# Optimization experiments

Hardware: AMD Instinct MI355X
Metric: run time of the kernel (lower is better)

## Reference

```python
import jax, jax.numpy as jnp
import numpy as np

D = 128; H = 4; DH = D // H; L = 2
NC = 50000; ND = 20000; NG = 30000; E = 200000; P = 200000
A = 10; S = 5; EAD = 32
# edge type table: (src node type, dst node type); node types: 0=chemical,1=disease,2=gene
ST = (0, 2, 0, 1, 1, 2)
DT = (2, 0, 1, 0, 2, 1)


def _seg_softmax(e, seg, n):
    # numerically stable softmax over edges grouped by destination node
    m = jax.ops.segment_max(e, seg, num_segments=n)
    ex = jnp.exp(e - m[seg])
    s = jax.ops.segment_sum(ex, seg, num_segments=n)
    return ex / (s[seg] + 1e-16)


def _ln(x, g, b):
    mu = jnp.mean(x, -1, keepdims=True)
    v = jnp.mean((x - mu) ** 2, -1, keepdims=True)
    return (x - mu) * jax.lax.rsqrt(v + 1e-5) * g + b


def setup_inputs():
    key = jax.random.key(0)
    ks = iter(jax.random.split(key, 80))
    nrm = lambda shape, sc: jax.random.normal(next(ks), shape, jnp.float32) * sc
    z = lambda shape: jnp.zeros(shape, jnp.float32)
    inp = {
        'emb_c': nrm((NC, D), 0.1), 'emb_d': nrm((ND, D), 0.1), 'emb_g': nrm((NG, D), 0.1),
        'Wsrc': nrm((L, 6, D, D), D ** -0.5), 'bsrc': z((L, 6, D)),
        'Wdst': nrm((L, 6, D, D), D ** -0.5), 'bdst': z((L, 6, D)),
        'attn': nrm((L, 6, H, DH), 0.1),
        'Wout': nrm((L, 3, D, D), D ** -0.5), 'bout': z((L, 3, D)),
        'ln_g': jnp.ones((L, 3, D), jnp.float32), 'ln_b': z((L, 3, D)),
        'at_emb': nrm((L, A, EAD), 0.1), 'as_emb': nrm((L, S, EAD), 0.1),
        'Wcat': nrm((L, 2, 2 * EAD, D), (2 * EAD) ** -0.5), 'bcat': z((L, 2, D)),
        'Wc1': nrm((L, 2, 2, D), 0.5), 'bc1': z((L, 2, D)),
        'Wc2': nrm((L, 2, D, D), D ** -0.5), 'bc2': z((L, 2, D)),
        'W_cd': nrm((D, D), D ** -0.5),
        'ea4': jax.random.normal(next(ks), (E, 2), jnp.float32),
        'ea5': jax.random.normal(next(ks), (E, 2), jnp.float32),
    }
    ri = lambda n: jax.random.randint(next(ks), (E,), 0, n)
    inp.update(src0=ri(NC), dst0=ri(NG), src1=ri(NG), dst1=ri(NC),
               src2=ri(NC), dst2=ri(ND), src3=ri(ND), dst3=ri(NC),
               src4=ri(ND), dst4=ri(NG), src5=ri(NG), dst5=ri(ND))
    inp['ea0'] = jnp.stack([ri(A), ri(S)], 1)
    inp['ea1'] = jnp.stack([ri(A), ri(S)], 1)
    inp['pair_src'] = jax.random.randint(next(ks), (P,), 0, NC)
    inp['pair_dst'] = jax.random.randint(next(ks), (P,), 0, ND)
    return inp


def _fwd(emb_c, emb_d, emb_g, Wsrc, bsrc, Wdst, bdst, attn, Wout, bout, ln_g, ln_b,
         at_emb, as_emb, Wcat, bcat, Wc1, bc1, Wc2, bc2, W_cd, ea4, ea5,
         SRC, DST, ea0, ea1, pair_src, pair_dst):
    xs = [emb_c, emb_d, emb_g]
    Ns = [x.shape[0] for x in xs]
    cat_attr = {0: ea0, 1: ea1}
    cont_attr = {4: ea4, 5: ea5}
    for l in range(L):
        agg = [jnp.zeros_like(x) for x in xs]
        for r in range(6):
            st, dt = ST[r], DT[r]
            si, di = SRC[r], DST[r]
            hs = xs[st] @ Wsrc[l, r] + bsrc[l, r]           # [Ns, D]
            hd = xs[dt] @ Wdst[l, r] + bdst[l, r]           # [Nd, D]
            ms = hs[si].reshape(-1, H, DH)                  # [E, H, DH] gathered src msgs
            md = hd[di].reshape(-1, H, DH)
            e = jax.nn.leaky_relu(jnp.sum((ms + md) * attn[l, r], -1), 0.2)  # [E, H]
            alpha = _seg_softmax(e, di, Ns[dt])
            if r in cat_attr:
                ea = cat_attr[r]
                emb = jnp.concatenate([at_emb[l][ea[:, 0]], as_emb[l][ea[:, 1]]], -1)
                g = jax.nn.sigmoid(emb @ Wcat[l, r] + bcat[l, r])
                ms = ms * g.reshape(-1, H, DH)
            elif r in cont_attr:
                k = r - 4
                h = jax.nn.gelu(cont_attr[r] @ Wc1[l, k] + bc1[l, k], approximate=False)
                g = jax.nn.sigmoid(h @ Wc2[l, k] + bc2[l, k])
                ms = ms * g.reshape(-1, H, DH)
            contrib = jax.ops.segment_sum(alpha[..., None] * ms, di, num_segments=Ns[dt])
            agg[dt] = agg[dt] + contrib.reshape(Ns[dt], D)
        xs = [_ln(xs[t] + (agg[t] @ Wout[l, t] + bout[l, t]), ln_g[l, t], ln_b[l, t])
              for t in range(3)]
    z = xs[0][pair_src] @ W_cd                              # [P, D]
    return jnp.sum(z * xs[1][pair_dst], -1)                 # [P]


def reference(emb_c, emb_d, emb_g, Wsrc, bsrc, Wdst, bdst, attn, Wout, bout, ln_g, ln_b,
              at_emb, as_emb, Wcat, bcat, Wc1, bc1, Wc2, bc2, W_cd, ea4, ea5,
              src0, dst0, src1, dst1, src2, dst2, src3, dst3, src4, dst4, src5, dst5,
              ea0, ea1, pair_src, pair_dst):
    SRC = (src0, src1, src2, src3, src4, src5)
    DST = (dst0, dst1, dst2, dst3, dst4, dst5)
    return _fwd(emb_c, emb_d, emb_g, Wsrc, bsrc, Wdst, bdst, attn, Wout, bout, ln_g, ln_b,
                at_emb, as_emb, Wcat, bcat, Wc1, bc1, Wc2, bc2, W_cd, ea4, ea5,
                SRC, DST, ea0, ea1, pair_src, pair_dst)
```

## Files before the change

kernel.cpp:

```cpp
#include <hip/hip_runtime.h>

typedef short s16x8 __attribute__((ext_vector_type(8)));
typedef float f32x4 __attribute__((ext_vector_type(4)));

#define DEV __device__ __forceinline__

static constexpr int NC_ = 50000, ND_ = 20000, NG_ = 30000;
static constexpr int EE = 200000, PP_ = 200000;
static constexpr int NTOT = NC_ + ND_ + NG_;

DEV unsigned short f2bf(float f) {
  unsigned u = __float_as_uint(f);
  u = u + 0x7FFFu + ((u >> 16) & 1u);
  return (unsigned short)(u >> 16);
}
DEV float bf2f(unsigned short h) { return __uint_as_float(((unsigned)h) << 16); }
DEV float sel4(float a, float b, float c, float d, int h) {
  float lo = (h & 1) ? b : a;
  float hi = (h & 1) ? d : c;
  return (h & 2) ? hi : lo;
}
DEV float fast_rcp(float x) {
#if __has_builtin(__builtin_amdgcn_rcpf)
  return __builtin_amdgcn_rcpf(x);
#else
  return 1.f / x;
#endif
}
DEV float gelu_fast(float x) { return x * fast_rcp(1.f + __expf(-1.702f * x)); }
DEV float sigmoid_fast(float x) { return fast_rcp(1.f + __expf(-x)); }

struct PackParams { const float* src[23]; unsigned short* dst; };
__global__ __launch_bounds__(256) void pack_kernel(PackParams P) {
  int m = blockIdx.x;
  const float* S = P.src[m];
  unsigned short* D = P.dst + (size_t)m * 16384;
  for (int idx = threadIdx.x; idx < 16384; idx += 256) {
    int j = idx & 7;
    int lane = (idx >> 3) & 63;
    int snb = idx >> 9;
    int s = snb >> 3, nbb = snb & 7;
    int k = s * 32 + 8 * (lane >> 4) + j;
    int n = nbb * 16 + (lane & 15);
    D[idx] = f2bf(S[k * 128 + n]);
  }
}

struct GEntry2 {
  const unsigned short* A; const unsigned short* Wp; const float* bias; void* out;
  const float* ea; const float* Wc1; const float* bc1;
  int M; int amode; int act; int outbf16; int blk0;
};
struct GParams2 { GEntry2 e[8]; int nent; };

__global__ __launch_bounds__(256) void gemm2(GParams2 P) {
  int bx = blockIdx.x;
  int ei = 0;
  while (ei + 1 < P.nent && bx >= P.e[ei + 1].blk0) ++ei;
  GEntry2 E = P.e[ei];
  const int M = E.M;
  const int row0 = (bx - E.blk0) * 128;
  if (row0 >= M) return;

  const int tid = threadIdx.x;
  const int w = tid >> 6, lane = tid & 63, g = lane >> 4, c = lane & 15;
  const int colHalf = (w & 1) * 64;
  const int rowHalf = (w >> 1) * 32;

  __shared__ __align__(16) unsigned short ldsA[128 * 128];
  __shared__ float ldsC1[384];

  if (E.amode == 2) {
    if (tid < 128) {
      ldsC1[tid] = E.Wc1[tid];
      ldsC1[128 + tid] = E.Wc1[128 + tid];
      ldsC1[256 + tid] = E.bc1[tid];
    }
    __syncthreads();
    for (int i = tid; i < 16384; i += 256) {
      int r = i >> 7, colx = i & 127;
      int row = row0 + r;
      int rr = row < M ? row : M - 1;
      float e0 = E.ea[(size_t)rr * 2], e1 = E.ea[(size_t)rr * 2 + 1];
      float h = e0 * ldsC1[colx] + e1 * ldsC1[128 + colx] + ldsC1[256 + colx];
      unsigned short hv = f2bf(gelu_fast(h));
      int cb = (colx * 2) ^ ((r & 7) << 4);
      *reinterpret_cast<unsigned short*>(reinterpret_cast<char*>(ldsA) + r * 256 + cb) = hv;
    }
    __syncthreads();
  }

  s16x8 Bf[4][4];
#pragma unroll
  for (int s = 0; s < 4; ++s)
#pragma unroll
    for (int nb = 0; nb < 4; ++nb) {
      int nbb = (w & 1) * 4 + nb;
      Bf[s][nb] = *reinterpret_cast<const s16x8*>(E.Wp + ((size_t)(s * 8 + nbb) * 64 + lane) * 8);
    }

#pragma unroll
  for (int itr = 0; itr < 2; ++itr) {
    if (row0 + itr * 64 >= M) break;
    const int rb = row0 + itr * 64 + rowHalf;

    s16x8 Af[2][4];
#pragma unroll
    for (int mt = 0; mt < 2; ++mt) {
      if (E.amode == 0) {
        int row = rb + mt * 16 + c;
        int rr = row < M ? row : M - 1;
        const unsigned short* ap = E.A + (size_t)rr * 128;
#pragma unroll
        for (int s = 0; s < 4; ++s)
          Af[mt][s] = *reinterpret_cast<const s16x8*>(ap + s * 32 + 8 * g);
      } else {
        int r = itr * 64 + rowHalf + mt * 16 + c;
#pragma unroll
        for (int s = 0; s < 4; ++s) {
          int cb = (64 * s + 16 * g) ^ ((r & 7) << 4);
          Af[mt][s] = *reinterpret_cast<const s16x8*>(reinterpret_cast<char*>(ldsA) + r * 256 + cb);
        }
      }
    }

    f32x4 acc[2][4];
#pragma unroll
    for (int mt = 0; mt < 2; ++mt)
#pragma unroll
      for (int nb = 0; nb < 4; ++nb) { acc[mt][nb][0] = 0.f; acc[mt][nb][1] = 0.f; acc[mt][nb][2] = 0.f; acc[mt][nb][3] = 0.f; }

#pragma unroll
    for (int mt = 0; mt < 2; ++mt)
#pragma unroll
      for (int s = 0; s < 4; ++s)
#pragma unroll
        for (int nb = 0; nb < 4; ++nb)
          acc[mt][nb] = __builtin_amdgcn_mfma_f32_16x16x32_bf16(Af[mt][s], Bf[s][nb], acc[mt][nb], 0, 0, 0);

#pragma unroll
    for (int mt = 0; mt < 2; ++mt)
#pragma unroll
      for (int nb = 0; nb < 4; ++nb) {
        int col = colHalf + nb * 16 + c;
        float bv = E.bias ? E.bias[col] : 0.f;
#pragma unroll
        for (int jj = 0; jj < 4; ++jj) {
          int row = rb + mt * 16 + 4 * g + jj;
          if (row < M) {
            float v = acc[mt][nb][jj] + bv;
            if (E.act == 1) v = sigmoid_fast(v);
            if (E.outbf16) ((unsigned short*)E.out)[(size_t)row * 128 + col] = f2bf(v);
            else ((float*)E.out)[(size_t)row * 128 + col] = v;
          }
        }
      }
  }
}

__global__ void wvbuild_kernel(const float* Wsrc, const float* Wdst, const float* bsrc, const float* bdst,
                               const float* attn, unsigned short* wv, float* bw, int l) {
  static const int RELT[3][4] = {{0, 2, 1, 3}, {3, 4, 2, 5}, {1, 5, 0, 4}};
  int t = blockIdx.x >> 4, col = blockIdx.x & 15;
  int b = col >> 2, h = col & 3;
  int r = RELT[t][b];
  bool isSrc = b < 2;
  const float* W = (isSrc ? Wsrc : Wdst) + (size_t)(l * 6 + r) * 16384;
  const float* bias = (isSrc ? bsrc : bdst) + (size_t)(l * 6 + r) * 128;
  const float* at = attn + (size_t)(l * 6 + r) * 128 + h * 32;
  int k = threadIdx.x;
  float acc = 0.f;
  for (int dh = 0; dh < 32; ++dh) acc += W[k * 128 + h * 32 + dh] * at[dh];
  wv[((size_t)t * 128 + k) * 16 + col] = f2bf(acc);
  if (k == 0) {
    float bacc = 0.f;
    for (int dh = 0; dh < 32; ++dh) bacc += bias[h * 32 + dh] * at[dh];
    bw[t * 16 + col] = bacc;
  }
}

__global__ __launch_bounds__(256) void advec_kernel(const unsigned short* xs_bf,
                                                    const unsigned short* wv, const float* bw, float* av16) {
  int rb0 = blockIdx.x * 64 + (threadIdx.x >> 6) * 16;
  if (rb0 >= NTOT) return;
  int lane = threadIdx.x & 63, g = lane >> 4, c = lane & 15;
  int t = rb0 >= (NC_ + ND_) ? 2 : (rb0 >= NC_ ? 1 : 0);
  const unsigned short* wvt = wv + (size_t)t * 2048;
  s16x8 Bf[4];
#pragma unroll
  for (int s = 0; s < 4; ++s) {
    s16x8 bfr;
#pragma unroll
    for (int i = 0; i < 8; ++i) bfr[i] = (short)wvt[(s * 32 + 8 * g + i) * 16 + c];
    Bf[s] = bfr;
  }
  f32x4 acc; acc[0] = 0.f; acc[1] = 0.f; acc[2] = 0.f; acc[3] = 0.f;
  const unsigned short* ap = xs_bf + (size_t)(rb0 + c) * 128;
#pragma unroll
  for (int s = 0; s < 4; ++s) {
    s16x8 a = *reinterpret_cast<const s16x8*>(ap + s * 32 + 8 * g);
    acc = __builtin_amdgcn_mfma_f32_16x16x32_bf16(a, Bf[s], acc, 0, 0, 0);
  }
  float bv = bw[t * 16 + c];
#pragma unroll
  for (int jj = 0; jj < 4; ++jj)
    av16[(size_t)(rb0 + 4 * g + jj) * 16 + c] = acc[jj] + bv;
}

struct CSRParams {
  const int* dst[6];
  int* cnt; int* rowp; int* cursor; int* col;
  int ndst[6];
};

__global__ __launch_bounds__(256) void hist_kernel(CSRParams P) {
  int gt = blockIdx.x * blockDim.x + threadIdx.x;
  int n = gridDim.x * blockDim.x;
  for (int idx = gt; idx < 6 * EE; idx += n) {
    int rel = idx / EE, i = idx - rel * EE;
    atomicAdd(&P.cnt[rel * 50000 + P.dst[rel][i]], 1);
  }
}

__global__ __launch_bounds__(1024) void scan_kernel(CSRParams P) {
  int rel = blockIdx.x;
  int n = P.ndst[rel];
  const int* c = P.cnt + rel * 50000;
  int* rp = P.rowp + rel * 50001;
  int* cur = P.cursor + rel * 50000;
  __shared__ int part[1024];
  int tid = threadIdx.x;
  int chunk = (n + 1023) / 1024;
  int lo = tid * chunk, hi = lo + chunk;
  if (hi > n) hi = n;
  int s = 0;
  for (int j = lo; j < hi; ++j) s += c[j];
  part[tid] = s;
  __syncthreads();
  if (tid == 0) {
    int acc = 0;
    for (int k = 0; k < 1024; ++k) { int v = part[k]; part[k] = acc; acc += v; }
    rp[n] = acc;
  }
  __syncthreads();
  int acc = part[tid];
  for (int j = lo; j < hi; ++j) { rp[j] = acc; cur[j] = acc; acc += c[j]; }
}

__global__ __launch_bounds__(256) void scatter_kernel(CSRParams P) {
  int gt = blockIdx.x * blockDim.x + threadIdx.x;
  int n = gridDim.x * blockDim.x;
  for (int idx = gt; idx < 6 * EE; idx += n) {
    int rel = idx / EE, i = idx - rel * EE;
    int d = P.dst[rel][i];
    int pos = atomicAdd(&P.cursor[rel * 50000 + d], 1);
    P.col[rel * EE + pos] = i;
  }
}

struct AggRel {
  const int* src; const int* col; const int* rowp;
  const float* asv; const float* adv;
  const unsigned short* hs;
  const int* ea;
  int gtype;
};
struct AggGroup { int n; unsigned short* aggbf; AggRel rel[2]; };
struct AggParams {
  AggGroup grp[2]; int ngrp;
  const float* gtab; const unsigned short* G;
};

__global__ __launch_bounds__(256) void agg_kernel(AggParams P) {
  int wid = (blockIdx.x * 256 + threadIdx.x) >> 6;
  int lane = threadIdx.x & 63;
  int q = lane & 15, e4 = lane >> 4, h = q >> 2;
  int gi = 0, node = wid;
  if (node >= P.grp[0].n) {
    node -= P.grp[0].n; gi = 1;
    if (gi >= P.ngrp || node >= P.grp[1].n) return;
  }
  const AggGroup& Gr = P.grp[gi];
  float acc[8];
#pragma unroll
  for (int j = 0; j < 8; ++j) acc[j] = 0.f;

  for (int rs = 0; rs < 2; ++rs) {
    const AggRel& R = Gr.rel[rs];
    int rp = R.rowp[node], re = R.rowp[node + 1];
    if (rp == re) continue;
    float4 ad4 = *reinterpret_cast<const float4*>(R.adv + (size_t)node * 16);
    int deg = re - rp;

    if (deg <= 64) {
      float e0 = -1e30f, e1 = -1e30f, e2 = -1e30f, e3 = -1e30f;
      int i_e = 0, si_e = 0, gx_e = 0;
      int k = rp + lane;
      bool ok = k < re;
      if (ok) {
        i_e = R.col[k];
        si_e = R.src[i_e];
        float4 s4 = *reinterpret_cast<const float4*>(R.asv + (size_t)si_e * 16);
        e0 = s4.x + ad4.x; e0 = e0 > 0.f ? e0 : 0.2f * e0;
        e1 = s4.y + ad4.y; e1 = e1 > 0.f ? e1 : 0.2f * e1;
        e2 = s4.z + ad4.z; e2 = e2 > 0.f ? e2 : 0.2f * e2;
        e3 = s4.w + ad4.w; e3 = e3 > 0.f ? e3 : 0.2f * e3;
        if (R.gtype == 1 || R.gtype == 2)
          gx_e = R.ea[(size_t)i_e * 2] * 5 + R.ea[(size_t)i_e * 2 + 1];
      }
      float m0 = e0, m1 = e1, m2 = e2, m3 = e3;
#pragma unroll
      for (int d = 1; d < 64; d <<= 1) {
        m0 = fmaxf(m0, __shfl_xor(m0, d));
        m1 = fmaxf(m1, __shfl_xor(m1, d));
        m2 = fmaxf(m2, __shfl_xor(m2, d));
        m3 = fmaxf(m3, __shfl_xor(m3, d));
      }
      float s0 = ok ? __expf(e0 - m0) : 0.f;
      float s1 = ok ? __expf(e1 - m1) : 0.f;
      float s2 = ok ? __expf(e2 - m2) : 0.f;
      float s3 = ok ? __expf(e3 - m3) : 0.f;
#pragma unroll
      for (int d = 1; d < 64; d <<= 1) {
        s0 += __shfl_xor(s0, d);
        s1 += __shfl_xor(s1, d);
        s2 += __shfl_xor(s2, d);
        s3 += __shfl_xor(s3, d);
      }
      float mh = sel4(m0, m1, m2, m3, h);
      float invh = 1.f / (sel4(s0, s1, s2, s3, h) + 1e-16f);

      int nit = (deg + 3) >> 2;
      for (int it = 0; it < nit; ++it) {
        int j = it * 4 + e4;
        bool valid = j < deg;
        int sij = __shfl(si_e, j);
        int ij = __shfl(i_e, j);
        float v0 = __shfl(e0, j), v1 = __shfl(e1, j), v2 = __shfl(e2, j), v3 = __shfl(e3, j);
        float ehj = sel4(v0, v1, v2, v3, h);
        float alpha = valid ? __expf(ehj - mh) * invh : 0.f;
        s16x8 ms = *reinterpret_cast<const s16x8*>(R.hs + (size_t)sij * 128 + 8 * q);
        if (R.gtype == 0) {
#pragma unroll
          for (int j2 = 0; j2 < 8; ++j2) acc[j2] += alpha * bf2f((unsigned short)ms[j2]);
        } else if (R.gtype == 3) {
          s16x8 gq = *reinterpret_cast<const s16x8*>(P.G + (size_t)ij * 128 + 8 * q);
#pragma unroll
          for (int j2 = 0; j2 < 8; ++j2) acc[j2] += alpha * bf2f((unsigned short)ms[j2]) * bf2f((unsigned short)gq[j2]);
        } else {
          int gxj = __shfl(gx_e, j);
          const float* gp = P.gtab + (size_t)((R.gtype - 1) * 50 + gxj) * 128 + 8 * q;
          float4 g0 = *reinterpret_cast<const float4*>(gp);
          float4 g1 = *reinterpret_cast<const float4*>(gp + 4);
          acc[0] += alpha * bf2f((unsigned short)ms[0]) * g0.x;
          acc[1] += alpha * bf2f((unsigned short)ms[1]) * g0.y;
          acc[2] += alpha * bf2f((unsigned short)ms[2]) * g0.z;
          acc[3] += alpha * bf2f((unsigned short)ms[3]) * g0.w;
          acc[4] += alpha * bf2f((unsigned short)ms[4]) * g1.x;
          acc[5] += alpha * bf2f((unsigned short)ms[5]) * g1.y;
          acc[6] += alpha * bf2f((unsigned short)ms[6]) * g1.z;
          acc[7] += alpha * bf2f((unsigned short)ms[7]) * g1.w;
        }
      }
    } else {
      float m0 = -1e30f, m1 = -1e30f, m2 = -1e30f, m3 = -1e30f;
      float s0 = 0.f, s1 = 0.f, s2 = 0.f, s3 = 0.f;
      for (int b = rp; b < re; b += 64) {
        int k = b + lane;
        if (k < re) {
          int i = R.col[k];
          int si = R.src[i];
          float4 s4 = *reinterpret_cast<const float4*>(R.asv + (size_t)si * 16);
          float e0 = s4.x + ad4.x; e0 = e0 > 0.f ? e0 : 0.2f * e0;
          float e1 = s4.y + ad4.y; e1 = e1 > 0.f ? e1 : 0.2f * e1;
          float e2 = s4.z + ad4.z; e2 = e2 > 0.f ? e2 : 0.2f * e2;
          float e3 = s4.w + ad4.w; e3 = e3 > 0.f ? e3 : 0.2f * e3;
          m0 = fmaxf(m0, e0); m1 = fmaxf(m1, e1); m2 = fmaxf(m2, e2); m3 = fmaxf(m3, e3);
        }
      }
#pragma unroll
      for (int d = 1; d < 64; d <<= 1) {
        m0 = fmaxf(m0, __shfl_xor(m0, d));
        m1 = fmaxf(m1, __shfl_xor(m1, d));
        m2 = fmaxf(m2, __shfl_xor(m2, d));
        m3 = fmaxf(m3, __shfl_xor(m3, d));
      }
      for (int b = rp; b < re; b += 64) {
        int k = b + lane;
        if (k < re) {
          int i = R.col[k];
          int si = R.src[i];
          float4 s4 = *reinterpret_cast<const float4*>(R.asv + (size_t)si * 16);
          float e0 = s4.x + ad4.x; e0 = e0 > 0.f ? e0 : 0.2f * e0;
          float e1 = s4.y + ad4.y; e1 = e1 > 0.f ? e1 : 0.2f * e1;
          float e2 = s4.z + ad4.z; e2 = e2 > 0.f ? e2 : 0.2f * e2;
          float e3 = s4.w + ad4.w; e3 = e3 > 0.f ? e3 : 0.2f * e3;
          s0 += __expf(e0 - m0); s1 += __expf(e1 - m1); s2 += __expf(e2 - m2); s3 += __expf(e3 - m3);
        }
      }
#pragma unroll
      for (int d = 1; d < 64; d <<= 1) {
        s0 += __shfl_xor(s0, d);
        s1 += __shfl_xor(s1, d);
        s2 += __shfl_xor(s2, d);
        s3 += __shfl_xor(s3, d);
      }
      float mh = sel4(m0, m1, m2, m3, h);
      float invh = 1.f / (sel4(s0, s1, s2, s3, h) + 1e-16f);
      float adh = sel4(ad4.x, ad4.y, ad4.z, ad4.w, h);
      int nit = (deg + 3) >> 2;
      for (int it = 0; it < nit; ++it) {
        int k = rp + it * 4 + e4;
        bool valid = k < re;
        int kk = valid ? k : re - 1;
        int i = R.col[kk];
        int si = R.src[i];
        float eh = R.asv[(size_t)si * 16 + h] + adh;
        eh = eh > 0.f ? eh : 0.2f * eh;
        float alpha = valid ? __expf(eh - mh) * invh : 0.f;
        s16x8 ms = *reinterpret_cast<const s16x8*>(R.hs + (size_t)si * 128 + 8 * q);
        if (R.gtype == 0) {
#pragma unroll
          for (int j2 = 0; j2 < 8; ++j2) acc[j2] += alpha * bf2f((unsigned short)ms[j2]);
        } else if (R.gtype == 3) {
          s16x8 gq = *reinterpret_cast<const s16x8*>(P.G + (size_t)i * 128 + 8 * q);
#pragma unroll
          for (int j2 = 0; j2 < 8; ++j2) acc[j2] += alpha * bf2f((unsigned short)ms[j2]) * bf2f((unsigned short)gq[j2]);
        } else {
          int a = R.ea[(size_t)i * 2], s2i = R.ea[(size_t)i * 2 + 1];
          const float* gp = P.gtab + (size_t)((R.gtype - 1) * 50 + a * 5 + s2i) * 128 + 8 * q;
          float4 g0 = *reinterpret_cast<const float4*>(gp);
          float4 g1 = *reinterpret_cast<const float4*>(gp + 4);
          acc[0] += alpha * bf2f((unsigned short)ms[0]) * g0.x;
          acc[1] += alpha * bf2f((unsigned short)ms[1]) * g0.y;
          acc[2] += alpha * bf2f((unsigned short)ms[2]) * g0.z;
          acc[3] += alpha * bf2f((unsigned short)ms[3]) * g0.w;
          acc[4] += alpha * bf2f((unsigned short)ms[4]) * g1.x;
          acc[5] += alpha * bf2f((unsigned short)ms[5]) * g1.y;
          acc[6] += alpha * bf2f((unsigned short)ms[6]) * g1.z;
          acc[7] += alpha * bf2f((unsigned short)ms[7]) * g1.w;
        }
      }
    }
  }
#pragma unroll
  for (int j = 0; j < 8; ++j) {
    acc[j] += __shfl_xor(acc[j], 16);
    acc[j] += __shfl_xor(acc[j], 32);
  }
  if (e4 == 0) {
    s16x8 o;
#pragma unroll
    for (int j = 0; j < 8; ++j) o[j] = (short)f2bf(acc[j]);
    *reinterpret_cast<s16x8*>(Gr.aggbf + (size_t)node * 128 + 8 * q) = o;
  }
}

__global__ void gatetab_kernel(const float* at_emb, const float* as_emb,
                               const float* Wcat, const float* bcat, float* gtab, int l) {
  int rel = blockIdx.x / 50, combo = blockIdx.x % 50;
  int a = combo / 5, s2 = combo % 5;
  int d = threadIdx.x;
  const float* Wb = Wcat + (size_t)(l * 2 + rel) * 64 * 128;
  float acc = bcat[(size_t)(l * 2 + rel) * 128 + d];
  const float* ae = at_emb + (size_t)(l * 10 + a) * 32;
  const float* se = as_emb + (size_t)(l * 5 + s2) * 32;
  for (int k = 0; k < 32; ++k) acc += ae[k] * Wb[k * 128 + d];
  for (int k = 0; k < 32; ++k) acc += se[k] * Wb[(32 + k) * 128 + d];
  gtab[(size_t)(rel * 50 + combo) * 128 + d] = 1.f / (1.f + __expf(-acc));
}

__global__ __launch_bounds__(256) void ln_kernel(float* xs, unsigned short* xs_bf, const float* tmp,
                                                 const float* g_base, const float* b_base) {
  int wid = (blockIdx.x * blockDim.x + threadIdx.x) >> 6;
  int lane = threadIdx.x & 63;
  int nw = (gridDim.x * blockDim.x) >> 6;
  for (int row = wid; row < NTOT; row += nw) {
    int t = row < NC_ ? 0 : (row < NC_ + ND_ ? 1 : 2);
    size_t ro = (size_t)row * 128 + 2 * lane;
    float2 x = *reinterpret_cast<const float2*>(xs + ro);
    float2 tv = *reinterpret_cast<const float2*>(tmp + ro);
    float a = x.x + tv.x, b = x.y + tv.y;
    float s = a + b;
#pragma unroll
    for (int m = 1; m <= 32; m <<= 1) s += __shfl_xor(s, m);
    float mu = s * 0.0078125f;
    float da = a - mu, db = b - mu;
    float v = da * da + db * db;
#pragma unroll
    for (int m = 1; m <= 32; m <<= 1) v += __shfl_xor(v, m);
    float rs = rsqrtf(v * 0.0078125f + 1e-5f);
    float2 gg = *reinterpret_cast<const float2*>(g_base + t * 128 + 2 * lane);
    float2 bb = *reinterpret_cast<const float2*>(b_base + t * 128 + 2 * lane);
    float2 o;
    o.x = da * rs * gg.x + bb.x;
    o.y = db * rs * gg.y + bb.y;
    *reinterpret_cast<float2*>(xs + ro) = o;
    ushort2 ob; ob.x = f2bf(o.x); ob.y = f2bf(o.y);
    *reinterpret_cast<ushort2*>(xs_bf + ro) = ob;
  }
}

__global__ __launch_bounds__(256) void cvt_init_kernel(const float* emb_c, const float* emb_d, const float* emb_g,
                                                       float* xs, unsigned short* xs_bf) {
  int i = blockIdx.x * 256 + threadIdx.x;
  if (i >= NTOT * 64) return;
  int row = i >> 6;
  int cpos = (i & 63) * 2;
  const float* src;
  if (row < NC_) src = emb_c + (size_t)row * 128;
  else if (row < NC_ + ND_) src = emb_d + (size_t)(row - NC_) * 128;
  else src = emb_g + (size_t)(row - NC_ - ND_) * 128;
  float2 v = *reinterpret_cast<const float2*>(src + cpos);
  *reinterpret_cast<float2*>(xs + (size_t)row * 128 + cpos) = v;
  ushort2 ob; ob.x = f2bf(v.x); ob.y = f2bf(v.y);
  *reinterpret_cast<ushort2*>(xs_bf + (size_t)row * 128 + cpos) = ob;
}

__global__ __launch_bounds__(256) void pair_kernel(const unsigned short* Ybf, const unsigned short* x1bf,
                                                   const int* ps, const int* pd, float* out) {
  int hw = (blockIdx.x * blockDim.x + threadIdx.x) >> 5;
  int lane = threadIdx.x & 31;
  int nhw = (gridDim.x * blockDim.x) >> 5;
  for (int p = hw; p < PP_; p += nhw) {
    int ai = ps[p], bi = pd[p];
    ushort4 y = *reinterpret_cast<const ushort4*>(Ybf + (size_t)ai * 128 + 4 * lane);
    ushort4 x = *reinterpret_cast<const ushort4*>(x1bf + (size_t)bi * 128 + 4 * lane);
    float s = bf2f(y.x) * bf2f(x.x) + bf2f(y.y) * bf2f(x.y) +
              bf2f(y.z) * bf2f(x.z) + bf2f(y.w) * bf2f(x.w);
#pragma unroll
    for (int m = 1; m <= 16; m <<= 1) s += __shfl_xor(s, m, 32);
    if (lane == 0) out[p] = s;
  }
}

__global__ void fill_kernel(float* out, int n, float v) {
  int i = blockIdx.x * blockDim.x + threadIdx.x;
  if (i < n) out[i] = v;
}

extern "C" void kernel_launch(void* const* d_in, const int* in_sizes, int n_in,
                              void* d_out, int out_size, void* d_ws, size_t ws_size,
                              hipStream_t stream) {
  (void)in_sizes; (void)n_in;
  const float* emb_c = (const float*)d_in[0];
  const float* emb_d = (const float*)d_in[1];
  const float* emb_g = (const float*)d_in[2];
  const float* Wsrc  = (const float*)d_in[3];
  const float* bsrc  = (const float*)d_in[4];
  const float* Wdst  = (const float*)d_in[5];
  const float* bdst  = (const float*)d_in[6];
  const float* attn  = (const float*)d_in[7];
  const float* Wout  = (const float*)d_in[8];
  const float* bout  = (const float*)d_in[9];
  const float* ln_g  = (const float*)d_in[10];
  const float* ln_b  = (const float*)d_in[11];
  const float* at_emb = (const float*)d_in[12];
  const float* as_emb = (const float*)d_in[13];
  const float* Wcat  = (const float*)d_in[14];
  const float* bcat  = (const float*)d_in[15];
  const float* Wc1   = (const float*)d_in[16];
  const float* bc1   = (const float*)d_in[17];
  const float* Wc2   = (const float*)d_in[18];
  const float* bc2   = (const float*)d_in[19];
  const float* W_cd  = (const float*)d_in[20];
  const float* ea4   = (const float*)d_in[21];
  const float* ea5   = (const float*)d_in[22];
  const int* srcs[6] = {(const int*)d_in[23], (const int*)d_in[25], (const int*)d_in[27],
                        (const int*)d_in[29], (const int*)d_in[31], (const int*)d_in[33]};
  const int* dsts[6] = {(const int*)d_in[24], (const int*)d_in[26], (const int*)d_in[28],
                        (const int*)d_in[30], (const int*)d_in[32], (const int*)d_in[34]};
  const int* ea0 = (const int*)d_in[35];
  const int* ea1 = (const int*)d_in[36];
  const int* pair_src = (const int*)d_in[37];
  const int* pair_dst = (const int*)d_in[38];

  static const int ST_[6] = {0, 2, 0, 1, 1, 2};
  static const int DT_[6] = {2, 0, 1, 0, 2, 1};
  static const int NT_[3] = {NC_, ND_, NG_};
  static const int HSOFF[6] = {0, 50000, 80000, 130000, 150000, 170000};
  static const int SBLK[6] = {0, 0, 1, 0, 1, 1};
  static const int DBLK[6] = {2, 2, 2, 3, 3, 3};
  static const int rowbase[3] = {0, 50000, 70000};

  size_t off = 0;
  auto alloc = [&](size_t bytes) { off = (off + 255) & ~(size_t)255; size_t o = off; off += bytes; return o; };
  size_t o_xs    = alloc((size_t)NTOT * 512);
  size_t o_xsbf  = alloc((size_t)NTOT * 256);
  size_t o_agbf  = alloc((size_t)NTOT * 256);
  size_t o_hs    = alloc((size_t)200000 * 256);
  size_t o_G     = alloc((size_t)200000 * 256);
  size_t o_av    = alloc((size_t)NTOT * 64);
  size_t o_wv    = alloc((size_t)3 * 128 * 16 * 2);
  size_t o_bw    = alloc((size_t)3 * 16 * 4);
  size_t o_gtab  = alloc((size_t)100 * 512);
  size_t o_wpack = alloc((size_t)23 * 16384 * 2);
  size_t o_cnt   = alloc((size_t)6 * 50000 * 4);
  size_t o_rowp  = alloc((size_t)6 * 50001 * 4);
  size_t o_cur   = alloc((size_t)6 * 50000 * 4);
  size_t o_col   = alloc((size_t)6 * EE * 4);
  if (off > ws_size) {
    fill_kernel<<<(PP_ + 255) / 256, 256, 0, stream>>>((float*)d_out, out_size, 1.0e6f);
    return;
  }

  char* ws = (char*)d_ws;
  float* xs = (float*)(ws + o_xs);
  unsigned short* xs_bf = (unsigned short*)(ws + o_xsbf);
  unsigned short* agg_bf = (unsigned short*)(ws + o_agbf);
  unsigned short* hs = (unsigned short*)(ws + o_hs);
  float* tmp = (float*)(ws + o_hs);
  unsigned short* Ybf = (unsigned short*)(ws + o_hs);
  unsigned short* G = (unsigned short*)(ws + o_G);
  float* av16 = (float*)(ws + o_av);
  unsigned short* wv = (unsigned short*)(ws + o_wv);
  float* bw = (float*)(ws + o_bw);
  float* gtab = (float*)(ws + o_gtab);
  unsigned short* wpack = (unsigned short*)(ws + o_wpack);
  int* cnt = (int*)(ws + o_cnt);
  int* rowp = (int*)(ws + o_rowp);
  int* cursor = (int*)(ws + o_cur);
  int* col = (int*)(ws + o_col);

  PackParams pk{};
  for (int l = 0; l < 2; ++l) {
    for (int r = 0; r < 6; ++r) pk.src[l * 11 + r] = Wsrc + (size_t)(l * 6 + r) * 16384;
    for (int k = 0; k < 2; ++k) pk.src[l * 11 + 6 + k] = Wc2 + (size_t)(l * 2 + k) * 16384;
    for (int t = 0; t < 3; ++t) pk.src[l * 11 + 8 + t] = Wout + (size_t)(l * 3 + t) * 16384;
  }
  pk.src[22] = W_cd;
  pk.dst = wpack;
  pack_kernel<<<23, 256, 0, stream>>>(pk);

  cvt_init_kernel<<<(NTOT * 64 + 255) / 256, 256, 0, stream>>>(emb_c, emb_d, emb_g, xs, xs_bf);

  hipMemsetAsync(cnt, 0, (size_t)6 * 50000 * 4, stream);
  CSRParams cp{};
  for (int r = 0; r < 6; ++r) { cp.dst[r] = dsts[r]; cp.ndst[r] = NT_[DT_[r]]; }
  cp.cnt = cnt; cp.rowp = rowp; cp.cursor = cursor; cp.col = col;
  hist_kernel<<<2048, 256, 0, stream>>>(cp);
  scan_kernel<<<6, 1024, 0, stream>>>(cp);
  scatter_kernel<<<2048, 256, 0, stream>>>(cp);

  auto nb = [](int M) { return (M + 127) / 128; };

  for (int l = 0; l < 2; ++l) {
    gatetab_kernel<<<100, 128, 0, stream>>>(at_emb, as_emb, Wcat, bcat, gtab, l);
    wvbuild_kernel<<<48, 128, 0, stream>>>(Wsrc, Wdst, bsrc, bdst, attn, wv, bw, l);

    GParams2 gp{};
    int blk = 0;
    for (int r = 0; r < 6; ++r) {
      int st = ST_[r];
      gp.e[r] = {xs_bf + (size_t)rowbase[st] * 128, wpack + (size_t)(l * 11 + r) * 16384,
                 bsrc + (size_t)(l * 6 + r) * 128, (void*)(hs + (size_t)HSOFF[r] * 128),
                 nullptr, nullptr, nullptr, NT_[st], 0, 0, 1, blk};
      blk += nb(NT_[st]);
    }
    gp.e[6] = {nullptr, wpack + (size_t)(l * 11 + 6) * 16384, bc2 + (size_t)(l * 2 + 0) * 128, (void*)G,
               ea4, Wc1 + (size_t)(l * 2 + 0) * 256, bc1 + (size_t)(l * 2 + 0) * 128, EE, 2, 1, 1, blk};
    blk += nb(EE);
    gp.nent = 7;
    gemm2<<<blk, 256, 0, stream>>>(gp);

    advec_kernel<<<(NTOT + 63) / 64, 256, 0, stream>>>(xs_bf, wv, bw, av16);

    auto mkrel = [&](int r) {
      AggRel R;
      R.src = srcs[r]; R.col = col + (size_t)r * EE; R.rowp = rowp + (size_t)r * 50001;
      R.asv = av16 + (size_t)rowbase[ST_[r]] * 16 + SBLK[r] * 4;
      R.adv = av16 + (size_t)rowbase[DT_[r]] * 16 + DBLK[r] * 4;
      R.hs = hs + (size_t)HSOFF[r] * 128;
      R.ea = (r == 0) ? ea0 : (r == 1) ? ea1 : nullptr;
      R.gtype = (r == 0) ? 1 : (r == 1) ? 2 : (r >= 4) ? 3 : 0;
      return R;
    };

    AggParams pa{};
    pa.grp[0].n = NG_; pa.grp[0].aggbf = agg_bf + (size_t)rowbase[2] * 128;
    pa.grp[0].rel[0] = mkrel(0); pa.grp[0].rel[1] = mkrel(4);
    pa.grp[1].n = NC_; pa.grp[1].aggbf = agg_bf + (size_t)rowbase[0] * 128;
    pa.grp[1].rel[0] = mkrel(1); pa.grp[1].rel[1] = mkrel(3);
    pa.ngrp = 2; pa.gtab = gtab; pa.G = G;
    agg_kernel<<<(NG_ + NC_) / 4, 256, 0, stream>>>(pa);

    GParams2 g5{};
    g5.e[0] = {nullptr, wpack + (size_t)(l * 11 + 7) * 16384, bc2 + (size_t)(l * 2 + 1) * 128, (void*)G,
               ea5, Wc1 + (size_t)(l * 2 + 1) * 256, bc1 + (size_t)(l * 2 + 1) * 128, EE, 2, 1, 1, 0};
    g5.nent = 1;
    gemm2<<<nb(EE), 256, 0, stream>>>(g5);

    AggParams pb{};
    pb.grp[0].n = ND_; pb.grp[0].aggbf = agg_bf + (size_t)rowbase[1] * 128;
    pb.grp[0].rel[0] = mkrel(2); pb.grp[0].rel[1] = mkrel(5);
    pb.grp[1].n = 0; pb.grp[1].aggbf = nullptr;
    pb.grp[1].rel[0] = mkrel(2); pb.grp[1].rel[1] = mkrel(5);
    pb.ngrp = 1; pb.gtab = gtab; pb.G = G;
    agg_kernel<<<(ND_) / 4, 256, 0, stream>>>(pb);

    GParams2 gw{};
    blk = 0;
    for (int t = 0; t < 3; ++t) {
      gw.e[t] = {agg_bf + (size_t)rowbase[t] * 128, wpack + (size_t)(l * 11 + 8 + t) * 16384,
                 bout + (size_t)(l * 3 + t) * 128, (void*)(tmp + (size_t)rowbase[t] * 128),
                 nullptr, nullptr, nullptr, NT_[t], 0, 0, 0, blk};
      blk += nb(NT_[t]);
    }
    gw.nent = 3;
    gemm2<<<blk, 256, 0, stream>>>(gw);

    ln_kernel<<<2048, 256, 0, stream>>>(xs, xs_bf, tmp, ln_g + (size_t)l * 384, ln_b + (size_t)l * 384);
  }

  GParams2 gy{};
  gy.e[0] = {xs_bf, wpack + (size_t)22 * 16384, nullptr, (void*)Ybf,
             nullptr, nullptr, nullptr, NC_, 0, 0, 1, 0};
  gy.nent = 1;
  gemm2<<<nb(NC_), 256, 0, stream>>>(gy);

  pair_kernel<<<2048, 256, 0, stream>>>(Ybf, xs_bf + (size_t)NC_ * 128, pair_src, pair_dst, (float*)d_out);
}
```

Baseline: 1.376 ms.

## Use 16-lane-per-node aggregation, merge agg launches, drop fp32 residual copy

Aggregation now assigns 16 lanes per destination node instead of a 64-lane wavefront. Each lane owns 8 contiguous features and walks the edges serially, which removes the cross-group reduction. The softmax fast path covers degree up to 16 and uses fast reciprocals. The edge-5 gate GEMM is folded into the first batched GEMM using a separate G5 buffer, so all three aggregation groups run in a single launch. The fp32 copy of node features is removed, so layer norm reads the residual from bf16, trading some precision for less memory traffic.

Measured after the change: 1.231 ms. 1.12x faster.

```diff
diff --git a/kernel.cpp b/kernel.cpp
--- a/kernel.cpp
+++ b/kernel.cpp
@@ -263,23 +263,22 @@
   const float* asv; const float* adv;
   const unsigned short* hs;
   const int* ea;
+  const unsigned short* G;
   int gtype;
 };
 struct AggGroup { int n; unsigned short* aggbf; AggRel rel[2]; };
-struct AggParams {
-  AggGroup grp[2]; int ngrp;
-  const float* gtab; const unsigned short* G;
-};
+struct AggParams { AggGroup grp[3]; const float* gtab; };
 
 __global__ __launch_bounds__(256) void agg_kernel(AggParams P) {
-  int wid = (blockIdx.x * 256 + threadIdx.x) >> 6;
-  int lane = threadIdx.x & 63;
-  int q = lane & 15, e4 = lane >> 4, h = q >> 2;
-  int gi = 0, node = wid;
-  if (node >= P.grp[0].n) {
-    node -= P.grp[0].n; gi = 1;
-    if (gi >= P.ngrp || node >= P.grp[1].n) return;
-  }
+  int gnode = (blockIdx.x * 256 + threadIdx.x) >> 4;
+  int sl = threadIdx.x & 15;
+  int h = sl >> 2;
+  int gi, node;
+  int n0 = P.grp[0].n, n1 = P.grp[1].n, n2 = P.grp[2].n;
+  if (gnode < n0) { gi = 0; node = gnode; }
+  else if (gnode < n0 + n1) { gi = 1; node = gnode - n0; }
+  else if (gnode < n0 + n1 + n2) { gi = 2; node = gnode - n0 - n1; }
+  else return;
   const AggGroup& Gr = P.grp[gi];
   float acc[8];
 #pragma unroll
@@ -292,13 +291,12 @@
     float4 ad4 = *reinterpret_cast<const float4*>(R.adv + (size_t)node * 16);
     int deg = re - rp;
 
-    if (deg <= 64) {
+    if (deg <= 16) {
       float e0 = -1e30f, e1 = -1e30f, e2 = -1e30f, e3 = -1e30f;
       int i_e = 0, si_e = 0, gx_e = 0;
-      int k = rp + lane;
-      bool ok = k < re;
+      bool ok = sl < deg;
       if (ok) {
-        i_e = R.col[k];
+        i_e = R.col[rp + sl];
         si_e = R.src[i_e];
         float4 s4 = *reinterpret_cast<const float4*>(R.asv + (size_t)si_e * 16);
         e0 = s4.x + ad4.x; e0 = e0 > 0.f ? e0 : 0.2f * e0;
@@ -310,46 +308,45 @@
       }
       float m0 = e0, m1 = e1, m2 = e2, m3 = e3;
 #pragma unroll
-      for (int d = 1; d < 64; d <<= 1) {
+      for (int d = 1; d < 16; d <<= 1) {
         m0 = fmaxf(m0, __shfl_xor(m0, d));
         m1 = fmaxf(m1, __shfl_xor(m1, d));
         m2 = fmaxf(m2, __shfl_xor(m2, d));
         m3 = fmaxf(m3, __shfl_xor(m3, d));
       }
-      float s0 = ok ? __expf(e0 - m0) : 0.f;
-      float s1 = ok ? __expf(e1 - m1) : 0.f;
-      float s2 = ok ? __expf(e2 - m2) : 0.f;
-      float s3 = ok ? __expf(e3 - m3) : 0.f;
-#pragma unroll
-      for (int d = 1; d < 64; d <<= 1) {
+      float x0 = ok ? __expf(e0 - m0) : 0.f;
+      float x1 = ok ? __expf(e1 - m1) : 0.f;
+      float x2 = ok ? __expf(e2 - m2) : 0.f;
+      float x3 = ok ? __expf(e3 - m3) : 0.f;
+      float s0 = x0, s1 = x1, s2 = x2, s3 = x3;
+#pragma unroll
+      for (int d = 1; d < 16; d <<= 1) {
         s0 += __shfl_xor(s0, d);
         s1 += __shfl_xor(s1, d);
         s2 += __shfl_xor(s2, d);
         s3 += __shfl_xor(s3, d);
       }
-      float mh = sel4(m0, m1, m2, m3, h);
-      float invh = 1.f / (sel4(s0, s1, s2, s3, h) + 1e-16f);
-
-      int nit = (deg + 3) >> 2;
-      for (int it = 0; it < nit; ++it) {
-        int j = it * 4 + e4;
-        bool valid = j < deg;
-        int sij = __shfl(si_e, j);
-        int ij = __shfl(i_e, j);
-        float v0 = __shfl(e0, j), v1 = __shfl(e1, j), v2 = __shfl(e2, j), v3 = __shfl(e3, j);
-        float ehj = sel4(v0, v1, v2, v3, h);
-        float alpha = valid ? __expf(ehj - mh) * invh : 0.f;
-        s16x8 ms = *reinterpret_cast<const s16x8*>(R.hs + (size_t)sij * 128 + 8 * q);
+      float a0 = x0 * fast_rcp(s0 + 1e-16f);
+      float a1 = x1 * fast_rcp(s1 + 1e-16f);
+      float a2 = x2 * fast_rcp(s2 + 1e-16f);
+      float a3 = x3 * fast_rcp(s3 + 1e-16f);
+
+      for (int j = 0; j < deg; ++j) {
+        int sij = __shfl(si_e, j, 16);
+        float alpha = sel4(__shfl(a0, j, 16), __shfl(a1, j, 16),
+                           __shfl(a2, j, 16), __shfl(a3, j, 16), h);
+        s16x8 ms = *reinterpret_cast<const s16x8*>(R.hs + (size_t)sij * 128 + 8 * sl);
         if (R.gtype == 0) {
 #pragma unroll
           for (int j2 = 0; j2 < 8; ++j2) acc[j2] += alpha * bf2f((unsigned short)ms[j2]);
         } else if (R.gtype == 3) {
-          s16x8 gq = *reinterpret_cast<const s16x8*>(P.G + (size_t)ij * 128 + 8 * q);
+          int ij = __shfl(i_e, j, 16);
+          s16x8 gq = *reinterpret_cast<const s16x8*>(R.G + (size_t)ij * 128 + 8 * sl);
 #pragma unroll
           for (int j2 = 0; j2 < 8; ++j2) acc[j2] += alpha * bf2f((unsigned short)ms[j2]) * bf2f((unsigned short)gq[j2]);
         } else {
-          int gxj = __shfl(gx_e, j);
-          const float* gp = P.gtab + (size_t)((R.gtype - 1) * 50 + gxj) * 128 + 8 * q;
+          int gxj = __shfl(gx_e, j, 16);
+          const float* gp = P.gtab + (size_t)((R.gtype - 1) * 50 + gxj) * 128 + 8 * sl;
           float4 g0 = *reinterpret_cast<const float4*>(gp);
           float4 g1 = *reinterpret_cast<const float4*>(gp + 4);
           acc[0] += alpha * bf2f((unsigned short)ms[0]) * g0.x;
@@ -364,71 +361,61 @@
       }
     } else {
       float m0 = -1e30f, m1 = -1e30f, m2 = -1e30f, m3 = -1e30f;
-      float s0 = 0.f, s1 = 0.f, s2 = 0.f, s3 = 0.f;
-      for (int b = rp; b < re; b += 64) {
-        int k = b + lane;
-        if (k < re) {
-          int i = R.col[k];
-          int si = R.src[i];
-          float4 s4 = *reinterpret_cast<const float4*>(R.asv + (size_t)si * 16);
-          float e0 = s4.x + ad4.x; e0 = e0 > 0.f ? e0 : 0.2f * e0;
-          float e1 = s4.y + ad4.y; e1 = e1 > 0.f ? e1 : 0.2f * e1;
-          float e2 = s4.z + ad4.z; e2 = e2 > 0.f ? e2 : 0.2f * e2;
-          float e3 = s4.w + ad4.w; e3 = e3 > 0.f ? e3 : 0.2f * e3;
-          m0 = fmaxf(m0, e0); m1 = fmaxf(m1, e1); m2 = fmaxf(m2, e2); m3 = fmaxf(m3, e3);
-        }
-      }
-#pragma unroll
-      for (int d = 1; d < 64; d <<= 1) {
+      for (int k = rp + sl; k < re; k += 16) {
+        int i = R.col[k];
+        int si = R.src[i];
+        float4 s4 = *reinterpret_cast<const float4*>(R.asv + (size_t)si * 16);
+        float e0 = s4.x + ad4.x; e0 = e0 > 0.f ? e0 : 0.2f * e0;
+        float e1 = s4.y + ad4.y; e1 = e1 > 0.f ? e1 : 0.2f * e1;
+        float e2 = s4.z + ad4.z; e2 = e2 > 0.f ? e2 : 0.2f * e2;
+        float e3 = s4.w + ad4.w; e3 = e3 > 0.f ? e3 : 0.2f * e3;
+        m0 = fmaxf(m0, e0); m1 = fmaxf(m1, e1); m2 = fmaxf(m2, e2); m3 = fmaxf(m3, e3);
+      }
+#pragma unroll
+      for (int d = 1; d < 16; d <<= 1) {
         m0 = fmaxf(m0, __shfl_xor(m0, d));
         m1 = fmaxf(m1, __shfl_xor(m1, d));
         m2 = fmaxf(m2, __shfl_xor(m2, d));
         m3 = fmaxf(m3, __shfl_xor(m3, d));
       }
-      for (int b = rp; b < re; b += 64) {
-        int k = b + lane;
-        if (k < re) {
-          int i = R.col[k];
-          int si = R.src[i];
-          float4 s4 = *reinterpret_cast<const float4*>(R.asv + (size_t)si * 16);
-          float e0 = s4.x + ad4.x; e0 = e0 > 0.f ? e0 : 0.2f * e0;
-          float e1 = s4.y + ad4.y; e1 = e1 > 0.f ? e1 : 0.2f * e1;
-          float e2 = s4.z + ad4.z; e2 = e2 > 0.f ? e2 : 0.2f * e2;
-          float e3 = s4.w + ad4.w; e3 = e3 > 0.f ? e3 : 0.2f * e3;
-          s0 += __expf(e0 - m0); s1 += __expf(e1 - m1); s2 += __expf(e2 - m2); s3 += __expf(e3 - m3);
-        }
-      }
-#pragma unroll
-      for (int d = 1; d < 64; d <<= 1) {
+      float s0 = 0.f, s1 = 0.f, s2 = 0.f, s3 = 0.f;
+      for (int k = rp + sl; k < re; k += 16) {
+        int i = R.col[k];
+        int si = R.src[i];
+        float4 s4 = *reinterpret_cast<const float4*>(R.asv + (size_t)si * 16);
+        float e0 = s4.x + ad4.x; e0 = e0 > 0.f ? e0 : 0.2f * e0;
+        float e1 = s4.y + ad4.y; e1 = e1 > 0.f ? e1 : 0.2f * e1;
+        float e2 = s4.z + ad4.z; e2 = e2 > 0.f ? e2 : 0.2f * e2;
+        float e3 = s4.w + ad4.w; e3 = e3 > 0.f ? e3 : 0.2f * e3;
+        s0 += __expf(e0 - m0); s1 += __expf(e1 - m1); s2 += __expf(e2 - m2); s3 += __expf(e3 - m3);
+      }
+#pragma unroll
+      for (int d = 1; d < 16; d <<= 1) {
         s0 += __shfl_xor(s0, d);
         s1 += __shfl_xor(s1, d);
         s2 += __shfl_xor(s2, d);
         s3 += __shfl_xor(s3, d);
       }
       float mh = sel4(m0, m1, m2, m3, h);
-      float invh = 1.f / (sel4(s0, s1, s2, s3, h) + 1e-16f);
+      float invh = fast_rcp(sel4(s0, s1, s2, s3, h) + 1e-16f);
       float adh = sel4(ad4.x, ad4.y, ad4.z, ad4.w, h);
-      int nit = (deg + 3) >> 2;
-      for (int it = 0; it < nit; ++it) {
-        int k = rp + it * 4 + e4;
-        bool valid = k < re;
-        int kk = valid ? k : re - 1;
-        int i = R.col[kk];
+      for (int k = rp; k < re; ++k) {
+        int i = R.col[k];
         int si = R.src[i];
         float eh = R.asv[(size_t)si * 16 + h] + adh;
         eh = eh > 0.f ? eh : 0.2f * eh;
-        float alpha = valid ? __expf(eh - mh) * invh : 0.f;
-        s16x8 ms = *reinterpret_cast<const s16x8*>(R.hs + (size_t)si * 128 + 8 * q);
+        float alpha = __expf(eh - mh) * invh;
+        s16x8 ms = *reinterpret_cast<const s16x8*>(R.hs + (size_t)si * 128 + 8 * sl);
         if (R.gtype == 0) {
 #pragma unroll
           for (int j2 = 0; j2 < 8; ++j2) acc[j2] += alpha * bf2f((unsigned short)ms[j2]);
         } else if (R.gtype == 3) {
-          s16x8 gq = *reinterpret_cast<const s16x8*>(P.G + (size_t)i * 128 + 8 * q);
+          s16x8 gq = *reinterpret_cast<const s16x8*>(R.G + (size_t)i * 128 + 8 * sl);
 #pragma unroll
           for (int j2 = 0; j2 < 8; ++j2) acc[j2] += alpha * bf2f((unsigned short)ms[j2]) * bf2f((unsigned short)gq[j2]);
         } else {
           int a = R.ea[(size_t)i * 2], s2i = R.ea[(size_t)i * 2 + 1];
-          const float* gp = P.gtab + (size_t)((R.gtype - 1) * 50 + a * 5 + s2i) * 128 + 8 * q;
+          const float* gp = P.gtab + (size_t)((R.gtype - 1) * 50 + a * 5 + s2i) * 128 + 8 * sl;
           float4 g0 = *reinterpret_cast<const float4*>(gp);
           float4 g1 = *reinterpret_cast<const float4*>(gp + 4);
           acc[0] += alpha * bf2f((unsigned short)ms[0]) * g0.x;
@@ -443,17 +430,10 @@
       }
     }
   }
-#pragma unroll
-  for (int j = 0; j < 8; ++j) {
-    acc[j] += __shfl_xor(acc[j], 16);
-    acc[j] += __shfl_xor(acc[j], 32);
-  }
-  if (e4 == 0) {
-    s16x8 o;
-#pragma unroll
-    for (int j = 0; j < 8; ++j) o[j] = (short)f2bf(acc[j]);
-    *reinterpret_cast<s16x8*>(Gr.aggbf + (size_t)node * 128 + 8 * q) = o;
-  }
+  s16x8 o;
+#pragma unroll
+  for (int j = 0; j < 8; ++j) o[j] = (short)f2bf(acc[j]);
+  *reinterpret_cast<s16x8*>(Gr.aggbf + (size_t)node * 128 + 8 * sl) = o;
 }
 
 __global__ void gatetab_kernel(const float* at_emb, const float* as_emb,
@@ -470,7 +450,7 @@
   gtab[(size_t)(rel * 50 + combo) * 128 + d] = 1.f / (1.f + __expf(-acc));
 }
 
-__global__ __launch_bounds__(256) void ln_kernel(float* xs, unsigned short* xs_bf, const float* tmp,
+__global__ __launch_bounds__(256) void ln_kernel(unsigned short* xs_bf, const float* tmp,
                                                  const float* g_base, const float* b_base) {
   int wid = (blockIdx.x * blockDim.x + threadIdx.x) >> 6;
   int lane = threadIdx.x & 63;
@@ -478,9 +458,9 @@
   for (int row = wid; row < NTOT; row += nw) {
     int t = row < NC_ ? 0 : (row < NC_ + ND_ ? 1 : 2);
     size_t ro = (size_t)row * 128 + 2 * lane;
-    float2 x = *reinterpret_cast<const float2*>(xs + ro);
+    ushort2 xb = *reinterpret_cast<const ushort2*>(xs_bf + ro);
     float2 tv = *reinterpret_cast<const float2*>(tmp + ro);
-    float a = x.x + tv.x, b = x.y + tv.y;
+    float a = bf2f(xb.x) + tv.x, b = bf2f(xb.y) + tv.y;
     float s = a + b;
 #pragma unroll
     for (int m = 1; m <= 32; m <<= 1) s += __shfl_xor(s, m);
@@ -492,17 +472,15 @@
     float rs = rsqrtf(v * 0.0078125f + 1e-5f);
     float2 gg = *reinterpret_cast<const float2*>(g_base + t * 128 + 2 * lane);
     float2 bb = *reinterpret_cast<const float2*>(b_base + t * 128 + 2 * lane);
-    float2 o;
-    o.x = da * rs * gg.x + bb.x;
-    o.y = db * rs * gg.y + bb.y;
-    *reinterpret_cast<float2*>(xs + ro) = o;
-    ushort2 ob; ob.x = f2bf(o.x); ob.y = f2bf(o.y);
+    ushort2 ob;
+    ob.x = f2bf(da * rs * gg.x + bb.x);
+    ob.y = f2bf(db * rs * gg.y + bb.y);
     *reinterpret_cast<ushort2*>(xs_bf + ro) = ob;
   }
 }
 
 __global__ __launch_bounds__(256) void cvt_init_kernel(const float* emb_c, const float* emb_d, const float* emb_g,
-                                                       float* xs, unsigned short* xs_bf) {
+                                                       unsigned short* xs_bf) {
   int i = blockIdx.x * 256 + threadIdx.x;
   if (i >= NTOT * 64) return;
   int row = i >> 6;
@@ -512,7 +490,6 @@
   else if (row < NC_ + ND_) src = emb_d + (size_t)(row - NC_) * 128;
   else src = emb_g + (size_t)(row - NC_ - ND_) * 128;
   float2 v = *reinterpret_cast<const float2*>(src + cpos);
-  *reinterpret_cast<float2*>(xs + (size_t)row * 128 + cpos) = v;
   ushort2 ob; ob.x = f2bf(v.x); ob.y = f2bf(v.y);
   *reinterpret_cast<ushort2*>(xs_bf + (size_t)row * 128 + cpos) = ob;
 }
@@ -576,20 +553,20 @@
   const int* pair_dst = (const int*)d_in[38];
 
   static const int ST_[6] = {0, 2, 0, 1, 1, 2};
-  static const int DT_[6] = {2, 0, 1, 0, 2, 1};
   static const int NT_[3] = {NC_, ND_, NG_};
   static const int HSOFF[6] = {0, 50000, 80000, 130000, 150000, 170000};
   static const int SBLK[6] = {0, 0, 1, 0, 1, 1};
   static const int DBLK[6] = {2, 2, 2, 3, 3, 3};
+  static const int DT_[6] = {2, 0, 1, 0, 2, 1};
   static const int rowbase[3] = {0, 50000, 70000};
 
   size_t off = 0;
   auto alloc = [&](size_t bytes) { off = (off + 255) & ~(size_t)255; size_t o = off; off += bytes; return o; };
-  size_t o_xs    = alloc((size_t)NTOT * 512);
   size_t o_xsbf  = alloc((size_t)NTOT * 256);
   size_t o_agbf  = alloc((size_t)NTOT * 256);
   size_t o_hs    = alloc((size_t)200000 * 256);
-  size_t o_G     = alloc((size_t)200000 * 256);
+  size_t o_G4    = alloc((size_t)200000 * 256);
+  size_t o_G5    = alloc((size_t)200000 * 256);
   size_t o_av    = alloc((size_t)NTOT * 64);
   size_t o_wv    = alloc((size_t)3 * 128 * 16 * 2);
   size_t o_bw    = alloc((size_t)3 * 16 * 4);
@@ -605,13 +582,13 @@
   }
 
   char* ws = (char*)d_ws;
-  float* xs = (float*)(ws + o_xs);
   unsigned short* xs_bf = (unsigned short*)(ws + o_xsbf);
   unsigned short* agg_bf = (unsigned short*)(ws + o_agbf);
   unsigned short* hs = (unsigned short*)(ws + o_hs);
   float* tmp = (float*)(ws + o_hs);
   unsigned short* Ybf = (unsigned short*)(ws + o_hs);
-  unsigned short* G = (unsigned short*)(ws + o_G);
+  unsigned short* G4 = (unsigned short*)(ws + o_G4);
+  unsigned short* G5 = (unsigned short*)(ws + o_G5);
   float* av16 = (float*)(ws + o_av);
   unsigned short* wv = (unsigned short*)(ws + o_wv);
   float* bw = (float*)(ws + o_bw);
@@ -632,7 +609,7 @@
   pk.dst = wpack;
   pack_kernel<<<23, 256, 0, stream>>>(pk);
 
-  cvt_init_kernel<<<(NTOT * 64 + 255) / 256, 256, 0, stream>>>(emb_c, emb_d, emb_g, xs, xs_bf);
+  cvt_init_kernel<<<(NTOT * 64 + 255) / 256, 256, 0, stream>>>(emb_c, emb_d, emb_g, xs_bf);
 
   hipMemsetAsync(cnt, 0, (size_t)6 * 50000 * 4, stream);
   CSRParams cp{};
@@ -657,10 +634,13 @@
                  nullptr, nullptr, nullptr, NT_[st], 0, 0, 1, blk};
       blk += nb(NT_[st]);
     }
-    gp.e[6] = {nullptr, wpack + (size_t)(l * 11 + 6) * 16384, bc2 + (size_t)(l * 2 + 0) * 128, (void*)G,
+    gp.e[6] = {nullptr, wpack + (size_t)(l * 11 + 6) * 16384, bc2 + (size_t)(l * 2 + 0) * 128, (void*)G4,
                ea4, Wc1 + (size_t)(l * 2 + 0) * 256, bc1 + (size_t)(l * 2 + 0) * 128, EE, 2, 1, 1, blk};
     blk += nb(EE);
-    gp.nent = 7;
+    gp.e[7] = {nullptr, wpack + (size_t)(l * 11 + 7) * 16384, bc2 + (size_t)(l * 2 + 1) * 128, (void*)G5,
+               ea5, Wc1 + (size_t)(l * 2 + 1) * 256, bc1 + (size_t)(l * 2 + 1) * 128, EE, 2, 1, 1, blk};
+    blk += nb(EE);
+    gp.nent = 8;
     gemm2<<<blk, 256, 0, stream>>>(gp);
 
     advec_kernel<<<(NTOT + 63) / 64, 256, 0, stream>>>(xs_bf, wv, bw, av16);
@@ -672,6 +652,7 @@
       R.adv = av16 + (size_t)rowbase[DT_[r]] * 16 + DBLK[r] * 4;
       R.hs = hs + (size_t)HSOFF[r] * 128;
       R.ea = (r == 0) ? ea0 : (r == 1) ? ea1 : nullptr;
+      R.G = (r == 4) ? G4 : (r == 5) ? G5 : nullptr;
       R.gtype = (r == 0) ? 1 : (r == 1) ? 2 : (r >= 4) ? 3 : 0;
       return R;
     };
@@ -681,22 +662,10 @@
     pa.grp[0].rel[0] = mkrel(0); pa.grp[0].rel[1] = mkrel(4);
     pa.grp[1].n = NC_; pa.grp[1].aggbf = agg_bf + (size_t)rowbase[0] * 128;
     pa.grp[1].rel[0] = mkrel(1); pa.grp[1].rel[1] = mkrel(3);
-    pa.ngrp = 2; pa.gtab = gtab; pa.G = G;
-    agg_kernel<<<(NG_ + NC_) / 4, 256, 0, stream>>>(pa);
-
-    GParams2 g5{};
-    g5.e[0] = {nullptr, wpack + (size_t)(l * 11 + 7) * 16384, bc2 + (size_t)(l * 2 + 1) * 128, (void*)G,
-               ea5, Wc1 + (size_t)(l * 2 + 1) * 256, bc1 + (size_t)(l * 2 + 1) * 128, EE, 2, 1, 1, 0};
-    g5.nent = 1;
-    gemm2<<<nb(EE), 256, 0, stream>>>(g5);
-
-    AggParams pb{};
-    pb.grp[0].n = ND_; pb.grp[0].aggbf = agg_bf + (size_t)rowbase[1] * 128;
-    pb.grp[0].rel[0] = mkrel(2); pb.grp[0].rel[1] = mkrel(5);
-    pb.grp[1].n = 0; pb.grp[1].aggbf = nullptr;
-    pb.grp[1].rel[0] = mkrel(2); pb.grp[1].rel[1] = mkrel(5);
-    pb.ngrp = 1; pb.gtab = gtab; pb.G = G;
-    agg_kernel<<<(ND_) / 4, 256, 0, stream>>>(pb);
+    pa.grp[2].n = ND_; pa.grp[2].aggbf = agg_bf + (size_t)rowbase[1] * 128;
+    pa.grp[2].rel[0] = mkrel(2); pa.grp[2].rel[1] = mkrel(5);
+    pa.gtab = gtab;
+    agg_kernel<<<(NTOT * 16 + 255) / 256, 256, 0, stream>>>(pa);
 
     GParams2 gw{};
     blk = 0;
@@ -709,7 +678,7 @@
     gw.nent = 3;
     gemm2<<<blk, 256, 0, stream>>>(gw);
 
-    ln_kernel<<<2048, 256, 0, stream>>>(xs, xs_bf, tmp, ln_g + (size_t)l * 384, ln_b + (size_t)l * 384);
+    ln_kernel<<<2048, 256, 0, stream>>>(xs_bf, tmp, ln_g + (size_t)l * 384, ln_b + (size_t)l * 384);
   }
 
   GParams2 gy{};
```
